# Performance work log

Measured on AMD Instinct MI355X. Metric: run time of the kernel, lower is better.

## Reference

```python
import jax, jax.numpy as jnp
import numpy as np
import math

EMBED = 1024
FF = 4096
HEADS = 16
HEAD = EMBED // HEADS
EPS = 1e-5


def new_gelu(x):
    c = math.sqrt(2.0 / math.pi)
    return 0.5 * x * (1.0 + jnp.tanh(c * (x + 0.044715 * x ** 3)))


def layer_norm(x, g, b):
    mu = jnp.mean(x, axis=-1, keepdims=True)
    var = jnp.var(x, axis=-1, keepdims=True)
    return (x - mu) * jax.lax.rsqrt(var + EPS) * g + b


def setup_inputs() -> dict:
    key = jax.random.key(0)
    ks = jax.random.split(key, 16)
    s = 0.02
    d = {
        'x': jax.random.normal(ks[0], (2, 2048, EMBED), jnp.float32),
        'Wq': jax.random.normal(ks[1], (EMBED, EMBED)) * s,
        'bq': jnp.zeros((EMBED,)),
        'Wk': jax.random.normal(ks[2], (EMBED, EMBED)) * s,
        'bk': jnp.zeros((EMBED,)),
        'Wv': jax.random.normal(ks[3], (EMBED, EMBED)) * s,
        'bv': jnp.zeros((EMBED,)),
        'Wp': jax.random.normal(ks[4], (EMBED, EMBED)) * s,
        'bp': jnp.zeros((EMBED,)),
        'W1': jax.random.normal(ks[5], (EMBED, FF)) * s,
        'b1': jnp.zeros((FF,)),
        'W2': jax.random.normal(ks[6], (FF, EMBED)) * s,
        'b2': jnp.zeros((EMBED,)),
        'g1': jnp.ones((EMBED,)), 'be1': jnp.zeros((EMBED,)),
        'g2': jnp.ones((EMBED,)), 'be2': jnp.zeros((EMBED,)),
    }
    return d


def reference(x, Wq, bq, Wk, bk, Wv, bv, Wp, bp, W1, b1, W2, b2, g1, be1, g2, be2):
    B, S, D = x.shape
    h = layer_norm(x, g1, be1)
    # project and split heads: [B,S,D] -> [B,H,S,Hd]
    def heads(y):
        return y.reshape(B, S, HEADS, HEAD).transpose(0, 2, 1, 3)
    Q = heads(h @ Wq + bq)
    K = heads(h @ Wk + bk)
    V = heads(h @ Wv + bv)
    att = jnp.einsum('bhqd,bhkd->bhqk', Q, K) / math.sqrt(HEAD)
    att = jax.nn.softmax(att, axis=-1)
    out = jnp.einsum('bhqk,bhkd->bhqd', att, V)
    out = out.transpose(0, 2, 1, 3).reshape(B, S, D)
    x = x + (out @ Wp + bp)  # dropout p=0 / eval -> identity
    h2 = layer_norm(x, g2, be2)
    x = x + (new_gelu(h2 @ W1 + b1) @ W2 + b2)
    return x
```

## Files before the change

### kernel.cpp

```cpp
#include <hip/hip_runtime.h>
#include <cstdint>


typedef __attribute__((ext_vector_type(8))) short short8;
typedef __attribute__((ext_vector_type(4))) float f32x4;

#define QSCL 0.18033688011112042f

__device__ __forceinline__ float bf2f(unsigned short u) {
    union { unsigned int i; float f; } v; v.i = ((unsigned int)u) << 16; return v.f;
}
__device__ __forceinline__ unsigned short f2bf(float f) {
    union { float f; unsigned int i; } v; v.f = f;
    unsigned int u = v.i;
    u += 0x7fff + ((u >> 16) & 1);
    return (unsigned short)(u >> 16);
}
__device__ __forceinline__ float gelu_f(float x) {
    float u = 0.7978845608028654f * (x + 0.044715f * x * x * x);
    float t = 1.f - 2.f / (__expf(2.f * u) + 1.f);
    return 0.5f * x * (1.f + t);
}

__device__ __forceinline__ void ln_dev(
    const float* __restrict__ x, const float* __restrict__ g,
    const float* __restrict__ b, unsigned short* __restrict__ o,
    int row, float* red)
{
    const int tid = threadIdx.x;
    const float4 v = ((const float4*)(x + (size_t)row * 1024))[tid];
    float f0 = v.x, f1 = v.y, f2 = v.z, f3 = v.w;
    float sum = f0 + f1 + f2 + f3;
    float sq  = f0 * f0 + f1 * f1 + f2 * f2 + f3 * f3;
    for (int off = 1; off < 64; off <<= 1) {
        sum += __shfl_xor(sum, off);
        sq  += __shfl_xor(sq,  off);
    }
    int wv = tid >> 6, ln = tid & 63;
    if (ln == 0) { red[wv] = sum; red[4 + wv] = sq; }
    __syncthreads();
    sum = red[0] + red[1] + red[2] + red[3];
    sq  = red[4] + red[5] + red[6] + red[7];
    float mu  = sum * (1.0f / 1024.0f);
    float var = sq  * (1.0f / 1024.0f) - mu * mu;
    float rsd = rsqrtf(fmaxf(var, 0.f) + 1e-5f);
    const float4 gg = ((const float4*)g)[tid];
    const float4 bb = ((const float4*)b)[tid];
    unsigned short* orow = o + (size_t)row * 1024;
    orow[4 * tid + 0] = f2bf((f0 - mu) * rsd * gg.x + bb.x);
    orow[4 * tid + 1] = f2bf((f1 - mu) * rsd * gg.y + bb.y);
    orow[4 * tid + 2] = f2bf((f2 - mu) * rsd * gg.z + bb.z);
    orow[4 * tid + 3] = f2bf((f3 - mu) * rsd * gg.w + bb.w);
}

__device__ __forceinline__ void transpose_dev(
    const float* __restrict__ in, unsigned short* __restrict__ out,
    int R, int C, int inStride, int bx, int by, unsigned short* tile ,
    float scale)
{
    const int tx = threadIdx.x & 15, ty = threadIdx.x >> 4;
    const int c0 = bx * 64, r0 = by * 64;
#pragma unroll
    for (int i = 0; i < 4; ++i) {
        int r = ty + 16 * i;
        float4 v = *(const float4*)(in + (size_t)(r0 + r) * inStride + c0 + tx * 4);
        tile[r * 70 + tx * 4 + 0] = f2bf(v.x * scale);
        tile[r * 70 + tx * 4 + 1] = f2bf(v.y * scale);
        tile[r * 70 + tx * 4 + 2] = f2bf(v.z * scale);
        tile[r * 70 + tx * 4 + 3] = f2bf(v.w * scale);
    }
    __syncthreads();
#pragma unroll
    for (int i = 0; i < 4; ++i) {
        int c = ty * 4 + i;
        ushort4 o;
        o.x = tile[(tx * 4 + 0) * 70 + c];
        o.y = tile[(tx * 4 + 1) * 70 + c];
        o.z = tile[(tx * 4 + 2) * 70 + c];
        o.w = tile[(tx * 4 + 3) * 70 + c];
        *(ushort4*)(out + (size_t)(c0 + c) * R + r0 + tx * 4) = o;
    }
}

__global__ __launch_bounds__(256) void ln_k(
    const float* __restrict__ x, const float* __restrict__ g,
    const float* __restrict__ b, unsigned short* __restrict__ o)
{
    __shared__ float red[8];
    ln_dev(x, g, b, o, blockIdx.x, red);
}
__global__ __launch_bounds__(256) void transpose_f2b(
    const float* __restrict__ in, unsigned short* __restrict__ out,
    int R, int C, int inStride, float scale)
{
    __shared__ unsigned short tile[64 * 70];
    transpose_dev(in, out, R, C, inStride, blockIdx.x, blockIdx.y, tile, scale);
}

__global__ __launch_bounds__(256) void prep1_k(
    const float* __restrict__ x,
    const float* __restrict__ g1, const float* __restrict__ be1,
    const float* __restrict__ Wq, const float* __restrict__ Wk,
    const float* __restrict__ Wv,
    const float* __restrict__ bq, const float* __restrict__ bk,
    const float* __restrict__ bv,
    unsigned short* __restrict__ hb,
    unsigned short* __restrict__ WTqkv,
    float* __restrict__ bcat)
{
    __shared__ unsigned short smem[64 * 70];
    const int b = blockIdx.x;
    if (b < 4096) {
        ln_dev(x, g1, be1, hb, b, (float*)smem);
    } else if (b < 4096 + 768) {
        int t = b - 4096;
        int w = t >> 8;
        int tt = t & 255;
        const float* W = (w == 0) ? Wq : (w == 1) ? Wk : Wv;
        transpose_dev(W, WTqkv + (size_t)w * 1024 * 1024,
                      1024, 1024, 1024, tt & 15, tt >> 4, smem,
                      (w == 0) ? QSCL : 1.f);
    } else {
        int i = (b - 4096 - 768) * 256 + threadIdx.x;
        float v = (i < 1024) ? bq[i] * QSCL : (i < 2048) ? bk[i - 1024] : bv[i - 2048];
        bcat[i] = v;
    }
}

__global__ __launch_bounds__(256) void prep2_k(
    const float* __restrict__ x1,
    const float* __restrict__ g2, const float* __restrict__ be2,
    const float* __restrict__ W1, const float* __restrict__ W2,
    unsigned short* __restrict__ h2,
    unsigned short* __restrict__ WT1,
    unsigned short* __restrict__ WT2)
{
    __shared__ unsigned short smem[64 * 70];
    const int b = blockIdx.x;
    if (b < 4096) {
        ln_dev(x1, g2, be2, h2, b, (float*)smem);
    } else if (b < 4096 + 1024) {
        int t = b - 4096;
        transpose_dev(W1, WT1, 1024, 4096, 4096, t & 63, t >> 6, smem, 1.f);
    } else {
        int t = b - 4096 - 1024;
        transpose_dev(W2, WT2, 4096, 1024, 1024, t & 15, t >> 4, smem, 1.f);
    }
}

__global__ __launch_bounds__(256) void vt_k(
    const unsigned short* __restrict__ src, int stride,
    unsigned short* __restrict__ Vt)
{
    __shared__ unsigned short tile[64][70];
    const int tx = threadIdx.x & 15, ty = threadIdx.x >> 4;
    const int t0 = blockIdx.x * 64;
    const int bh = blockIdx.y;
    const int bo = (bh >> 4) * 2048;
    const int ho = (bh & 15) * 64;
    const unsigned short* s = src + (size_t)bo * stride + ho;
#pragma unroll
    for (int i = 0; i < 4; ++i) {
        int r = ty + 16 * i;
        ushort4 v = *(const ushort4*)(s + (size_t)(t0 + r) * stride + tx * 4);
        tile[r][tx * 4 + 0] = v.x;
        tile[r][tx * 4 + 1] = v.y;
        tile[r][tx * 4 + 2] = v.z;
        tile[r][tx * 4 + 3] = v.w;
    }
    __syncthreads();
    unsigned short* dst = Vt + (size_t)bh * 64 * 2048;
    const int hh = tx >> 3;
    const int uu = (tx & 7) * 2;
#pragma unroll
    for (int i = 0; i < 4; ++i) {
        int d = ty * 4 + i;
        ushort4 o;
        o.x = tile[32 * hh + uu][d];
        o.y = tile[32 * hh + 16 + uu][d];
        o.z = tile[32 * hh + uu + 1][d];
        o.w = tile[32 * hh + 17 + uu][d];
        *(ushort4*)(dst + (size_t)d * 2048 + t0 + tx * 4) = o;
    }
}

__global__ __launch_bounds__(512, 4) void gemm5(
    const unsigned short* __restrict__ A,
    const unsigned short* __restrict__ Bt,
    const float* __restrict__ bias,
    const float* __restrict__ res,
    void* __restrict__ C,
    int M, int N, int K, int ldb, int dogelu, int out32, float bscale)
{
    __shared__ unsigned short sA[2][128 * 68];
    __shared__ unsigned short sB[2][128 * 68];
    const int tid  = threadIdx.x;
    const int wave = tid >> 6;
    const int lane = tid & 63;
    const int quad = lane >> 4;
    const int l15  = lane & 15;
    const int bm = blockIdx.y * 128;
    const int bn = blockIdx.x * 128;
    const int wM = (wave & 1) * 64;
    const int wN = (wave >> 1) * 32;

    f32x4 acc[4][2];
#pragma unroll
    for (int i = 0; i < 4; ++i)
#pragma unroll
        for (int j = 0; j < 2; ++j)
            acc[i][j] = (f32x4){0.f, 0.f, 0.f, 0.f};

    const int rowS = tid >> 3;
    const int kcS  = (tid & 7) * 8;
    const unsigned short* gA  = A  + (size_t)(bm + rowS) * K + kcS;
    const unsigned short* gA2 = gA + (size_t)64 * K;
    const unsigned short* gB  = Bt + (size_t)(bn + rowS) * ldb + kcS;
    const unsigned short* gB2 = gB + (size_t)64 * ldb;
    const int lo1 = rowS * 68 + kcS;
    const int lo2 = (rowS + 64) * 68 + kcS;

    const int nt = K >> 6;
    *(short8*)(&sA[0][lo1]) = *(const short8*)(gA);
    *(short8*)(&sA[0][lo2]) = *(const short8*)(gA2);
    *(short8*)(&sB[0][lo1]) = *(const short8*)(gB);
    *(short8*)(&sB[0][lo2]) = *(const short8*)(gB2);
    short8 ar1 = *(const short8*)(gA + 64);
    short8 ar2 = *(const short8*)(gA2 + 64);
    short8 br1 = *(const short8*)(gB + 64);
    short8 br2 = *(const short8*)(gB2 + 64);

    for (int t = 0; t < nt; ++t) {
        const int buf = t & 1;
        __syncthreads();

        short8 aF[4], bF[2];
#pragma unroll
        for (int mi = 0; mi < 4; ++mi)
            aF[mi] = *(const short8*)(&sA[buf][(wM + mi * 16 + l15) * 68 + quad * 8]);
#pragma unroll
        for (int ni = 0; ni < 2; ++ni)
            bF[ni] = *(const short8*)(&sB[buf][(wN + ni * 16 + l15) * 68 + quad * 8]);

        if (t + 1 < nt) {
            *(short8*)(&sA[buf ^ 1][lo1]) = ar1;
            *(short8*)(&sA[buf ^ 1][lo2]) = ar2;
            *(short8*)(&sB[buf ^ 1][lo1]) = br1;
            *(short8*)(&sB[buf ^ 1][lo2]) = br2;
            if (t + 2 < nt) {
                const int k2 = (t + 2) << 6;
                ar1 = *(const short8*)(gA + k2);
                ar2 = *(const short8*)(gA2 + k2);
                br1 = *(const short8*)(gB + k2);
                br2 = *(const short8*)(gB2 + k2);
            }
        }

        __builtin_amdgcn_s_setprio(1);
#pragma unroll
        for (int mi = 0; mi < 4; ++mi)
#pragma unroll
            for (int ni = 0; ni < 2; ++ni)
                acc[mi][ni] = __builtin_amdgcn_mfma_f32_16x16x32_bf16(
                    aF[mi], bF[ni], acc[mi][ni], 0, 0, 0);
        __builtin_amdgcn_s_setprio(0);

#pragma unroll
        for (int mi = 0; mi < 4; ++mi)
            aF[mi] = *(const short8*)(&sA[buf][(wM + mi * 16 + l15) * 68 + 32 + quad * 8]);
#pragma unroll
        for (int ni = 0; ni < 2; ++ni)
            bF[ni] = *(const short8*)(&sB[buf][(wN + ni * 16 + l15) * 68 + 32 + quad * 8]);

        __builtin_amdgcn_s_setprio(1);
#pragma unroll
        for (int mi = 0; mi < 4; ++mi)
#pragma unroll
            for (int ni = 0; ni < 2; ++ni)
                acc[mi][ni] = __builtin_amdgcn_mfma_f32_16x16x32_bf16(
                    aF[mi], bF[ni], acc[mi][ni], 0, 0, 0);
        __builtin_amdgcn_s_setprio(0);
    }

#pragma unroll
    for (int ni = 0; ni < 2; ++ni) {
        int col = bn + wN + ni * 16 + l15;
        float bv = bias ? bias[col] * bscale : 0.f;
#pragma unroll
        for (int mi = 0; mi < 4; ++mi) {
            int row = bm + wM + mi * 16 + quad * 4;
#pragma unroll
            for (int r = 0; r < 4; ++r) {
                float v = acc[mi][ni][r] + bv;
                if (dogelu) v = gelu_f(v);
                size_t idx = (size_t)(row + r) * N + col;
                if (res) v += res[idx];
                if (out32) ((float*)C)[idx] = v;
                else       ((unsigned short*)C)[idx] = f2bf(v);
            }
        }
    }
}

__global__ __launch_bounds__(512, 1) void attn_k(
    const unsigned short* __restrict__ Q,
    const unsigned short* __restrict__ K,
    const unsigned short* __restrict__ Vt,
    unsigned short* __restrict__ O, int qs)
{
    __shared__ unsigned short smem[67584];
    unsigned short* sK = smem;
    unsigned short* sV = smem + 4 * 5632;
    unsigned short* sP = smem + 8 * 5632;

    const int tid  = threadIdx.x;
    const int wave = tid >> 6;
    const int g    = wave & 3;
    const int h    = wave >> 2;
    const int lane = tid & 63;
    const int quad = lane >> 4;
    const int l15  = lane & 15;
    const int bh = blockIdx.x * 4 + (blockIdx.y & 3);
    const int qb = (blockIdx.y >> 2) * 256;
    const int bo = (bh >> 4) * 2048;
    const int ho = (bh & 15) * 64;

    const unsigned short* Qb  = Q  + (size_t)bo * qs + ho;
    const unsigned short* Kb  = K  + (size_t)bo * qs + ho;
    const unsigned short* Vtb = Vt + (size_t)bh * 64 * 2048;
    unsigned short* sPg = sP + g * 5632;
    const int ni0 = 2 * h;

    short8 qF[2][4];
#pragma unroll
    for (int ks = 0; ks < 2; ++ks)
#pragma unroll
        for (int mi = 0; mi < 4; ++mi)
            qF[ks][mi] = *(const short8*)(Qb +
                (size_t)(qb + g * 64 + mi * 16 + l15) * qs + ks * 32 + quad * 8);

    short8 onesF;
#pragma unroll
    for (int j = 0; j < 8; ++j) onesF[j] = (short)0x3F80;

    f32x4 accO[4][4];
    f32x4 accL[4];
#pragma unroll
    for (int mi = 0; mi < 4; ++mi) {
        accL[mi] = (f32x4){0.f, 0.f, 0.f, 0.f};
#pragma unroll
        for (int nd = 0; nd < 4; ++nd) accO[mi][nd] = (f32x4){0.f, 0.f, 0.f, 0.f};
    }

    const int rowS = tid >> 3;
    const int dcS  = (tid & 7) * 8;

    short8 kr[2], vr[2];
#pragma unroll
    for (int s = 0; s < 2; ++s) {
        kr[s] = *(const short8*)(Kb + (size_t)(s * 64 + rowS) * qs + dcS);
        vr[s] = *(const short8*)(Vtb + (size_t)rowS * 2048 + s * 64 + dcS);
    }
#pragma unroll
    for (int s = 0; s < 2; ++s) {
        *(short8*)(sK + s * 5632 + rowS * 88 + dcS) = kr[s];
        *(short8*)(sV + s * 5632 + rowS * 88 + dcS) = vr[s];
    }
#pragma unroll
    for (int s = 0; s < 2; ++s) {
        kr[s] = *(const short8*)(Kb + (size_t)(128 + s * 64 + rowS) * qs + dcS);
        vr[s] = *(const short8*)(Vtb + (size_t)rowS * 2048 + 128 + s * 64 + dcS);
    }

    for (int kt = 0; kt < 2048; kt += 128) {
        const int buf = (kt >> 7) & 1;
        __syncthreads();

#pragma unroll
        for (int s = 0; s < 2; ++s) {
            const unsigned short* sKb = sK + (buf * 2 + s) * 5632;
            const unsigned short* sVb = sV + (buf * 2 + s) * 5632;

            short8 bK[2][2];
#pragma unroll
            for (int ks = 0; ks < 2; ++ks)
#pragma unroll
                for (int nj = 0; nj < 2; ++nj)
                    bK[ks][nj] = *(const short8*)(sKb +
                        ((ni0 + nj) * 16 + l15) * 88 + ks * 32 + quad * 8);

            f32x4 s0[4], s1[4];
#pragma unroll
            for (int mi = 0; mi < 4; ++mi) {
                s0[mi] = (f32x4){0.f, 0.f, 0.f, 0.f};
                s1[mi] = s0[mi];
#pragma unroll
                for (int ks = 0; ks < 2; ++ks) {
                    s0[mi] = __builtin_amdgcn_mfma_f32_16x16x32_bf16(qF[ks][mi], bK[ks][0], s0[mi], 0, 0, 0);
                    s1[mi] = __builtin_amdgcn_mfma_f32_16x16x32_bf16(qF[ks][mi], bK[ks][1], s1[mi], 0, 0, 0);
                }
            }

            if (s == 0 && kt + 128 < 2048) {
#pragma unroll
                for (int u = 0; u < 2; ++u) {
                    *(short8*)(sK + ((buf ^ 1) * 2 + u) * 5632 + rowS * 88 + dcS) = kr[u];
                    *(short8*)(sV + ((buf ^ 1) * 2 + u) * 5632 + rowS * 88 + dcS) = vr[u];
                }
                if (kt + 256 < 2048) {
#pragma unroll
                    for (int u = 0; u < 2; ++u) {
                        kr[u] = *(const short8*)(Kb + (size_t)(kt + 256 + u * 64 + rowS) * qs + dcS);
                        vr[u] = *(const short8*)(Vtb + (size_t)rowS * 2048 + kt + 256 + u * 64 + dcS);
                    }
                }
            }

#pragma unroll
            for (int mi = 0; mi < 4; ++mi)
#pragma unroll
                for (int r = 0; r < 4; ++r) {
                    float p0 = __builtin_amdgcn_exp2f(s0[mi][r]);
                    float p1 = __builtin_amdgcn_exp2f(s1[mi][r]);
                    unsigned int w;
                    asm("v_cvt_pk_bf16_f32 %0, %1, %2" : "=v"(w) : "v"(p0), "v"(p1));
                    *(unsigned int*)(sPg + (mi * 16 + quad * 4 + r) * 88 + h * 32 + l15 * 2) = w;
                }

            short8 aP[4], bV[4];
#pragma unroll
            for (int nd = 0; nd < 4; ++nd)
                bV[nd] = *(const short8*)(sVb + (nd * 16 + l15) * 88 + h * 32 + quad * 8);
#pragma unroll
            for (int mi = 0; mi < 4; ++mi)
                aP[mi] = *(const short8*)(sPg + (mi * 16 + l15) * 88 + h * 32 + quad * 8);

            __builtin_amdgcn_s_setprio(1);
#pragma unroll
            for (int mi = 0; mi < 4; ++mi) {
#pragma unroll
                for (int nd = 0; nd < 4; ++nd)
                    accO[mi][nd] = __builtin_amdgcn_mfma_f32_16x16x32_bf16(
                        aP[mi], bV[nd], accO[mi][nd], 0, 0, 0);
                accL[mi] = __builtin_amdgcn_mfma_f32_16x16x32_bf16(
                    aP[mi], onesF, accL[mi], 0, 0, 0);
            }
            __builtin_amdgcn_s_setprio(0);
        }
    }

    __syncthreads();
    float* scr = (float*)smem;
    float* po = scr + (size_t)(g * 64 + lane) * 68;
    float* pl = scr + 17408 + (size_t)(g * 64 + lane) * 20;
    if (h == 1) {
#pragma unroll
        for (int mi = 0; mi < 4; ++mi) {
#pragma unroll
            for (int nd = 0; nd < 4; ++nd)
                *(f32x4*)(po + mi * 16 + nd * 4) = accO[mi][nd];
            *(f32x4*)(pl + mi * 4) = accL[mi];
        }
    }
    __syncthreads();
    if (h == 0) {
#pragma unroll
        for (int mi = 0; mi < 4; ++mi) {
            accL[mi] += *(const f32x4*)(pl + mi * 4);
#pragma unroll
            for (int nd = 0; nd < 4; ++nd)
                accO[mi][nd] += *(const f32x4*)(po + mi * 16 + nd * 4);
        }
#pragma unroll
        for (int mi = 0; mi < 4; ++mi)
#pragma unroll
            for (int r = 0; r < 4; ++r) {
                int row = qb + g * 64 + mi * 16 + quad * 4 + r;
                float inv = 1.f / accL[mi][r];
#pragma unroll
                for (int nd = 0; nd < 4; ++nd)
                    O[(size_t)(bo + row) * 1024 + ho + nd * 16 + l15] =
                        f2bf(accO[mi][nd][r] * inv);
            }
    }
}

extern "C" void kernel_launch(void* const* d_in, const int* in_sizes, int n_in,
                              void* d_out, int out_size, void* d_ws, size_t ws_size,
                              hipStream_t stream)
{
    (void)in_sizes; (void)n_in; (void)out_size;
    const float* x   = (const float*)d_in[0];
    const float* Wq  = (const float*)d_in[1];
    const float* bq  = (const float*)d_in[2];
    const float* Wk  = (const float*)d_in[3];
    const float* bk  = (const float*)d_in[4];
    const float* Wv  = (const float*)d_in[5];
    const float* bv  = (const float*)d_in[6];
    const float* Wp  = (const float*)d_in[7];
    const float* bp  = (const float*)d_in[8];
    const float* W1  = (const float*)d_in[9];
    const float* b1  = (const float*)d_in[10];
    const float* W2  = (const float*)d_in[11];
    const float* b2  = (const float*)d_in[12];
    const float* g1  = (const float*)d_in[13];
    const float* be1 = (const float*)d_in[14];
    const float* g2  = (const float*)d_in[15];
    const float* be2 = (const float*)d_in[16];
    float* out = (float*)d_out;

    char* ws = (char*)d_ws;
    char* dob = (char*)d_out;
    const size_t MB = 1024 * 1024;

    if (ws_size >= 40 * MB) {
        unsigned short* hb    = (unsigned short*)dob;
        unsigned short* WTqkv = (unsigned short*)(dob + 8 * MB);
        float*          bcat  = (float*)(dob + 14 * MB);
        unsigned short* QKV   = (unsigned short*)ws;
        unsigned short* att   = (unsigned short*)(ws + 24 * MB);
        unsigned short* Vt    = (unsigned short*)(ws + 32 * MB);
        unsigned short* WTp   = (unsigned short*)(ws + 32 * MB);
        unsigned short* h2    = (unsigned short*)ws;
        unsigned short* WT1   = (unsigned short*)(ws + 8 * MB);
        unsigned short* WT2   = (unsigned short*)(ws + 16 * MB);
        unsigned short* act   = (unsigned short*)(ws + 24 * MB);

        prep1_k<<<4096 + 768 + 12, 256, 0, stream>>>(
            x, g1, be1, Wq, Wk, Wv, bq, bk, bv, hb, WTqkv, bcat);
        gemm5<<<dim3(24, 32), 512, 0, stream>>>(hb, WTqkv, bcat, nullptr, QKV,
                                                4096, 3072, 1024, 1024, 0, 0, 1.f);
        vt_k<<<dim3(32, 32), 256, 0, stream>>>(QKV + 2048, 3072, Vt);
        attn_k<<<dim3(8, 32), 512, 0, stream>>>(QKV, QKV + 1024, Vt, att, 3072);
        transpose_f2b<<<dim3(16, 16), 256, 0, stream>>>(Wp, WTp, 1024, 1024, 1024, 1.f);
        gemm5<<<dim3(8, 32), 512, 0, stream>>>(att, WTp, bp, x, out,
                                               4096, 1024, 1024, 1024, 0, 1, 1.f);
        prep2_k<<<4096 + 2048, 256, 0, stream>>>(out, g2, be2, W1, W2, h2, WT1, WT2);
        for (int c = 0; c < 2; ++c) {
            gemm5<<<dim3(16, 32), 512, 0, stream>>>(h2, WT1 + (size_t)c * 2048 * 1024,
                                                    b1 + c * 2048, nullptr, act,
                                                    4096, 2048, 1024, 1024, 1, 0, 1.f);
            gemm5<<<dim3(8, 32), 512, 0, stream>>>(act, WT2 + (size_t)c * 2048,
                                                   c == 0 ? b2 : nullptr, out, out,
                                                   4096, 1024, 2048, 4096, 0, 1, 1.f);
        }
    } else {
        unsigned short* Qw  = (unsigned short*)(ws);
        unsigned short* Kw  = (unsigned short*)(ws + 8 * MB);
        unsigned short* Vw  = (unsigned short*)(ws + 16 * MB);
        unsigned short* hb  = (unsigned short*)dob;
        unsigned short* WTq = (unsigned short*)(dob + 8 * MB);
        unsigned short* VtF = (unsigned short*)(dob + 8 * MB);
        unsigned short* att = Qw;
        unsigned short* WTb = Kw;
        unsigned short* h2  = Vw;
        unsigned short* act = Qw;

        ln_k<<<4096, 256, 0, stream>>>(x, g1, be1, hb);
        transpose_f2b<<<dim3(16, 16), 256, 0, stream>>>(Wq, WTq, 1024, 1024, 1024, QSCL);
        gemm5<<<dim3(8, 32), 512, 0, stream>>>(hb, WTq, bq, nullptr, Qw, 4096, 1024, 1024, 1024, 0, 0, QSCL);
        transpose_f2b<<<dim3(16, 16), 256, 0, stream>>>(Wk, WTq, 1024, 1024, 1024, 1.f);
        gemm5<<<dim3(8, 32), 512, 0, stream>>>(hb, WTq, bk, nullptr, Kw, 4096, 1024, 1024, 1024, 0, 0, 1.f);
        transpose_f2b<<<dim3(16, 16), 256, 0, stream>>>(Wv, WTq, 1024, 1024, 1024, 1.f);
        gemm5<<<dim3(8, 32), 512, 0, stream>>>(hb, WTq, bv, nullptr, Vw, 4096, 1024, 1024, 1024, 0, 0, 1.f);
        vt_k<<<dim3(32, 32), 256, 0, stream>>>(Vw, 1024, VtF);
        attn_k<<<dim3(8, 32), 512, 0, stream>>>(Qw, Kw, VtF, att, 1024);
        transpose_f2b<<<dim3(16, 16), 256, 0, stream>>>(Wp, WTb, 1024, 1024, 1024, 1.f);
        gemm5<<<dim3(8, 32), 512, 0, stream>>>(att, WTb, bp, x, out, 4096, 1024, 1024, 1024, 0, 1, 1.f);
        ln_k<<<4096, 256, 0, stream>>>(out, g2, be2, h2);
        for (int c = 0; c < 4; ++c) {
            transpose_f2b<<<dim3(16, 16), 256, 0, stream>>>(W1 + c * 1024, WTb, 1024, 1024, 4096, 1.f);
            gemm5<<<dim3(8, 32), 512, 0, stream>>>(h2, WTb, b1 + c * 1024, nullptr, act,
                                                   4096, 1024, 1024, 1024, 1, 0, 1.f);
            unsigned short* WT2c = WTb + 1024 * 1024;
            transpose_f2b<<<dim3(16, 16), 256, 0, stream>>>(W2 + (size_t)c * 1024 * 1024, WT2c,
                                                            1024, 1024, 1024, 1.f);
            gemm5<<<dim3(8, 32), 512, 0, stream>>>(act, WT2c, c == 0 ? b2 : nullptr,
                                                   out, out, 4096, 1024, 1024, 1024, 0, 1, 1.f);
        }
    }
}
```

Before: 366.4 us.

## Add 256-thread GEMM with 64x64 per-wave tiles for QKV and FC1

Introduces a gemm6 kernel that uses 4 waves of 256 threads, each computing a 64x64 sub-tile of the 128x128 block with 16 MFMA accumulators, and a K-step of 32 with register-prefetched double buffering. It replaces gemm5 for the QKV projection and the first FFN GEMM. The intent is more MFMA work per LDS fragment load and less shared memory per block, which improves reuse. In exchange each wave holds more accumulator registers, and the smaller K-step means more barriers per unit of work.

```diff
diff --git a/kernel.cpp b/kernel.cpp
--- a/kernel.cpp
+++ b/kernel.cpp
@@ -181,6 +181,108 @@
         o.z = tile[32 * hh + uu + 1][d];
         o.w = tile[32 * hh + 17 + uu][d];
         *(ushort4*)(dst + (size_t)d * 2048 + t0 + tx * 4) = o;
+    }
+}
+
+__global__ __launch_bounds__(256, 3) void gemm6(
+    const unsigned short* __restrict__ A,
+    const unsigned short* __restrict__ Bt,
+    const float* __restrict__ bias,
+    const float* __restrict__ res,
+    void* __restrict__ C,
+    int M, int N, int K, int ldb, int dogelu, int out32, float bscale)
+{
+    __shared__ unsigned short sA[2][128 * 34];
+    __shared__ unsigned short sB[2][128 * 34];
+    const int tid  = threadIdx.x;
+    const int wave = tid >> 6;
+    const int lane = tid & 63;
+    const int quad = lane >> 4;
+    const int l15  = lane & 15;
+    const int bm = blockIdx.y * 128;
+    const int bn = blockIdx.x * 128;
+    const int wM = (wave & 1) * 64;
+    const int wN = (wave >> 1) * 64;
+
+    f32x4 acc[4][4];
+#pragma unroll
+    for (int i = 0; i < 4; ++i)
+#pragma unroll
+        for (int j = 0; j < 4; ++j)
+            acc[i][j] = (f32x4){0.f, 0.f, 0.f, 0.f};
+
+    const int rowS = tid >> 2;
+    const int kcS  = (tid & 3) * 8;
+    const unsigned short* gA  = A  + (size_t)(bm + rowS) * K + kcS;
+    const unsigned short* gA2 = gA + (size_t)64 * K;
+    const unsigned short* gB  = Bt + (size_t)(bn + rowS) * ldb + kcS;
+    const unsigned short* gB2 = gB + (size_t)64 * ldb;
+    const int lo1 = rowS * 34 + kcS;
+    const int lo2 = (rowS + 64) * 34 + kcS;
+
+    const int np = K >> 5;
+    *(short8*)(&sA[0][lo1]) = *(const short8*)(gA);
+    *(short8*)(&sA[0][lo2]) = *(const short8*)(gA2);
+    *(short8*)(&sB[0][lo1]) = *(const short8*)(gB);
+    *(short8*)(&sB[0][lo2]) = *(const short8*)(gB2);
+    short8 ar1 = *(const short8*)(gA + 32);
+    short8 ar2 = *(const short8*)(gA2 + 32);
+    short8 br1 = *(const short8*)(gB + 32);
+    short8 br2 = *(const short8*)(gB2 + 32);
+
+    for (int p = 0; p < np; ++p) {
+        const int buf = p & 1;
+        __syncthreads();
+
+        short8 aF[4], bF[4];
+#pragma unroll
+        for (int mi = 0; mi < 4; ++mi)
+            aF[mi] = *(const short8*)(&sA[buf][(wM + mi * 16 + l15) * 34 + quad * 8]);
+#pragma unroll
+        for (int ni = 0; ni < 4; ++ni)
+            bF[ni] = *(const short8*)(&sB[buf][(wN + ni * 16 + l15) * 34 + quad * 8]);
+
+        if (p + 1 < np) {
+            *(short8*)(&sA[buf ^ 1][lo1]) = ar1;
+            *(short8*)(&sA[buf ^ 1][lo2]) = ar2;
+            *(short8*)(&sB[buf ^ 1][lo1]) = br1;
+            *(short8*)(&sB[buf ^ 1][lo2]) = br2;
+            if (p + 2 < np) {
+                const int k2 = (p + 2) << 5;
+                ar1 = *(const short8*)(gA + k2);
+                ar2 = *(const short8*)(gA2 + k2);
+                br1 = *(const short8*)(gB + k2);
+                br2 = *(const short8*)(gB2 + k2);
+            }
+        }
+
+        __builtin_amdgcn_s_setprio(1);
+#pragma unroll
+        for (int mi = 0; mi < 4; ++mi)
+#pragma unroll
+            for (int ni = 0; ni < 4; ++ni)
+                acc[mi][ni] = __builtin_amdgcn_mfma_f32_16x16x32_bf16(
+                    aF[mi], bF[ni], acc[mi][ni], 0, 0, 0);
+        __builtin_amdgcn_s_setprio(0);
+    }
+
+#pragma unroll
+    for (int ni = 0; ni < 4; ++ni) {
+        int col = bn + wN + ni * 16 + l15;
+        float bv = bias ? bias[col] * bscale : 0.f;
+#pragma unroll
+        for (int mi = 0; mi < 4; ++mi) {
+            int row = bm + wM + mi * 16 + quad * 4;
+#pragma unroll
+            for (int r = 0; r < 4; ++r) {
+                float v = acc[mi][ni][r] + bv;
+                if (dogelu) v = gelu_f(v);
+                size_t idx = (size_t)(row + r) * N + col;
+                if (res) v += res[idx];
+                if (out32) ((float*)C)[idx] = v;
+                else       ((unsigned short*)C)[idx] = f2bf(v);
+            }
+        }
     }
 }
 
@@ -528,7 +630,7 @@
 
         prep1_k<<<4096 + 768 + 12, 256, 0, stream>>>(
             x, g1, be1, Wq, Wk, Wv, bq, bk, bv, hb, WTqkv, bcat);
-        gemm5<<<dim3(24, 32), 512, 0, stream>>>(hb, WTqkv, bcat, nullptr, QKV,
+        gemm6<<<dim3(24, 32), 256, 0, stream>>>(hb, WTqkv, bcat, nullptr, QKV,
                                                 4096, 3072, 1024, 1024, 0, 0, 1.f);
         vt_k<<<dim3(32, 32), 256, 0, stream>>>(QKV + 2048, 3072, Vt);
         attn_k<<<dim3(8, 32), 512, 0, stream>>>(QKV, QKV + 1024, Vt, att, 3072);
@@ -537,7 +639,7 @@
                                                4096, 1024, 1024, 1024, 0, 1, 1.f);
         prep2_k<<<4096 + 2048, 256, 0, stream>>>(out, g2, be2, W1, W2, h2, WT1, WT2);
         for (int c = 0; c < 2; ++c) {
-            gemm5<<<dim3(16, 32), 512, 0, stream>>>(h2, WT1 + (size_t)c * 2048 * 1024,
+            gemm6<<<dim3(16, 32), 256, 0, stream>>>(h2, WT1 + (size_t)c * 2048 * 1024,
                                                     b1 + c * 2048, nullptr, act,
                                                     4096, 2048, 1024, 1024, 1, 0, 1.f);
             gemm5<<<dim3(8, 32), 512, 0, stream>>>(act, WT2 + (size_t)c * 2048,
```

Result: slower. 398.1 us (+8.6%).

## Split K across wave pairs in GEMM with larger per-wave tiles and LDS reduction

Applied to the files above, without the earlier changes.

Reorganizes the GEMM so each wave computes a 64x64 output tile on one half of each 64-wide K slice, instead of a 64x32 tile over the full slice. The two K-halves are summed through shared memory before the epilogue. This raises MFMA work per LDS fragment load and improves operand reuse. In exchange it doubles the accumulator registers per wave, adds an LDS reduction with extra barriers, and leaves half the waves idle during the epilogue.

```diff
diff --git a/kernel.cpp b/kernel.cpp
--- a/kernel.cpp
+++ b/kernel.cpp
@@ -184,7 +184,7 @@
     }
 }
 
-__global__ __launch_bounds__(512, 4) void gemm5(
+__global__ __launch_bounds__(512, 4) void gemm7(
     const unsigned short* __restrict__ A,
     const unsigned short* __restrict__ Bt,
     const float* __restrict__ bias,
@@ -196,19 +196,22 @@
     __shared__ unsigned short sB[2][128 * 68];
     const int tid  = threadIdx.x;
     const int wave = tid >> 6;
+    const int q    = wave & 3;
+    const int s    = wave >> 2;
     const int lane = tid & 63;
     const int quad = lane >> 4;
     const int l15  = lane & 15;
     const int bm = blockIdx.y * 128;
     const int bn = blockIdx.x * 128;
-    const int wM = (wave & 1) * 64;
-    const int wN = (wave >> 1) * 32;
-
-    f32x4 acc[4][2];
+    const int wM = (q & 1) * 64;
+    const int wN = (q >> 1) * 64;
+    const int pofs = s * 32;
+
+    f32x4 acc[4][4];
 #pragma unroll
     for (int i = 0; i < 4; ++i)
 #pragma unroll
-        for (int j = 0; j < 2; ++j)
+        for (int j = 0; j < 4; ++j)
             acc[i][j] = (f32x4){0.f, 0.f, 0.f, 0.f};
 
     const int rowS = tid >> 3;
@@ -234,13 +237,13 @@
         const int buf = t & 1;
         __syncthreads();
 
-        short8 aF[4], bF[2];
+        short8 aF[4], bF[4];
 #pragma unroll
         for (int mi = 0; mi < 4; ++mi)
-            aF[mi] = *(const short8*)(&sA[buf][(wM + mi * 16 + l15) * 68 + quad * 8]);
-#pragma unroll
-        for (int ni = 0; ni < 2; ++ni)
-            bF[ni] = *(const short8*)(&sB[buf][(wN + ni * 16 + l15) * 68 + quad * 8]);
+            aF[mi] = *(const short8*)(&sA[buf][(wM + mi * 16 + l15) * 68 + pofs + quad * 8]);
+#pragma unroll
+        for (int ni = 0; ni < 4; ++ni)
+            bF[ni] = *(const short8*)(&sB[buf][(wN + ni * 16 + l15) * 68 + pofs + quad * 8]);
 
         if (t + 1 < nt) {
             *(short8*)(&sA[buf ^ 1][lo1]) = ar1;
@@ -260,43 +263,42 @@
 #pragma unroll
         for (int mi = 0; mi < 4; ++mi)
 #pragma unroll
-            for (int ni = 0; ni < 2; ++ni)
+            for (int ni = 0; ni < 4; ++ni)
                 acc[mi][ni] = __builtin_amdgcn_mfma_f32_16x16x32_bf16(
                     aF[mi], bF[ni], acc[mi][ni], 0, 0, 0);
         __builtin_amdgcn_s_setprio(0);
-
+    }
+
+    __syncthreads();
+    float* base = (q < 2) ? (float*)&sA[0][0] : (float*)&sB[0][0];
+    float* slot = base + (size_t)((q & 1) * 64 + lane) * 65;
+    if (s == 1) {
 #pragma unroll
         for (int mi = 0; mi < 4; ++mi)
-            aF[mi] = *(const short8*)(&sA[buf][(wM + mi * 16 + l15) * 68 + 32 + quad * 8]);
-#pragma unroll
-        for (int ni = 0; ni < 2; ++ni)
-            bF[ni] = *(const short8*)(&sB[buf][(wN + ni * 16 + l15) * 68 + 32 + quad * 8]);
-
-        __builtin_amdgcn_s_setprio(1);
-#pragma unroll
-        for (int mi = 0; mi < 4; ++mi)
-#pragma unroll
-            for (int ni = 0; ni < 2; ++ni)
-                acc[mi][ni] = __builtin_amdgcn_mfma_f32_16x16x32_bf16(
-                    aF[mi], bF[ni], acc[mi][ni], 0, 0, 0);
-        __builtin_amdgcn_s_setprio(0);
-    }
-
-#pragma unroll
-    for (int ni = 0; ni < 2; ++ni) {
-        int col = bn + wN + ni * 16 + l15;
-        float bv = bias ? bias[col] * bscale : 0.f;
-#pragma unroll
-        for (int mi = 0; mi < 4; ++mi) {
-            int row = bm + wM + mi * 16 + quad * 4;
-#pragma unroll
-            for (int r = 0; r < 4; ++r) {
-                float v = acc[mi][ni][r] + bv;
-                if (dogelu) v = gelu_f(v);
-                size_t idx = (size_t)(row + r) * N + col;
-                if (res) v += res[idx];
-                if (out32) ((float*)C)[idx] = v;
-                else       ((unsigned short*)C)[idx] = f2bf(v);
+#pragma unroll
+            for (int ni = 0; ni < 4; ++ni)
+#pragma unroll
+                for (int r = 0; r < 4; ++r)
+                    slot[mi * 16 + ni * 4 + r] = acc[mi][ni][r];
+    }
+    __syncthreads();
+    if (s == 0) {
+#pragma unroll
+        for (int ni = 0; ni < 4; ++ni) {
+            int col = bn + wN + ni * 16 + l15;
+            float bv = bias ? bias[col] * bscale : 0.f;
+#pragma unroll
+            for (int mi = 0; mi < 4; ++mi) {
+                int row = bm + wM + mi * 16 + quad * 4;
+#pragma unroll
+                for (int r = 0; r < 4; ++r) {
+                    float v = acc[mi][ni][r] + slot[mi * 16 + ni * 4 + r] + bv;
+                    if (dogelu) v = gelu_f(v);
+                    size_t idx = (size_t)(row + r) * N + col;
+                    if (res) v += res[idx];
+                    if (out32) ((float*)C)[idx] = v;
+                    else       ((unsigned short*)C)[idx] = f2bf(v);
+                }
             }
         }
     }
@@ -528,19 +530,19 @@
 
         prep1_k<<<4096 + 768 + 12, 256, 0, stream>>>(
             x, g1, be1, Wq, Wk, Wv, bq, bk, bv, hb, WTqkv, bcat);
-        gemm5<<<dim3(24, 32), 512, 0, stream>>>(hb, WTqkv, bcat, nullptr, QKV,
+        gemm7<<<dim3(24, 32), 512, 0, stream>>>(hb, WTqkv, bcat, nullptr, QKV,
                                                 4096, 3072, 1024, 1024, 0, 0, 1.f);
         vt_k<<<dim3(32, 32), 256, 0, stream>>>(QKV + 2048, 3072, Vt);
         attn_k<<<dim3(8, 32), 512, 0, stream>>>(QKV, QKV + 1024, Vt, att, 3072);
         transpose_f2b<<<dim3(16, 16), 256, 0, stream>>>(Wp, WTp, 1024, 1024, 1024, 1.f);
-        gemm5<<<dim3(8, 32), 512, 0, stream>>>(att, WTp, bp, x, out,
+        gemm7<<<dim3(8, 32), 512, 0, stream>>>(att, WTp, bp, x, out,
                                                4096, 1024, 1024, 1024, 0, 1, 1.f);
         prep2_k<<<4096 + 2048, 256, 0, stream>>>(out, g2, be2, W1, W2, h2, WT1, WT2);
         for (int c = 0; c < 2; ++c) {
-            gemm5<<<dim3(16, 32), 512, 0, stream>>>(h2, WT1 + (size_t)c * 2048 * 1024,
+            gemm7<<<dim3(16, 32), 512, 0, stream>>>(h2, WT1 + (size_t)c * 2048 * 1024,
                                                     b1 + c * 2048, nullptr, act,
                                                     4096, 2048, 1024, 1024, 1, 0, 1.f);
-            gemm5<<<dim3(8, 32), 512, 0, stream>>>(act, WT2 + (size_t)c * 2048,
+            gemm7<<<dim3(8, 32), 512, 0, stream>>>(act, WT2 + (size_t)c * 2048,
                                                    c == 0 ? b2 : nullptr, out, out,
                                                    4096, 1024, 2048, 4096, 0, 1, 1.f);
         }
@@ -558,24 +560,24 @@
 
         ln_k<<<4096, 256, 0, stream>>>(x, g1, be1, hb);
         transpose_f2b<<<dim3(16, 16), 256, 0, stream>>>(Wq, WTq, 1024, 1024, 1024, QSCL);
-        gemm5<<<dim3(8, 32), 512, 0, stream>>>(hb, WTq, bq, nullptr, Qw, 4096, 1024, 1024, 1024, 0, 0, QSCL);
+        gemm7<<<dim3(8, 32), 512, 0, stream>>>(hb, WTq, bq, nullptr, Qw, 4096, 1024, 1024, 1024, 0, 0, QSCL);
         transpose_f2b<<<dim3(16, 16), 256, 0, stream>>>(Wk, WTq, 1024, 1024, 1024, 1.f);
-        gemm5<<<dim3(8, 32), 512, 0, stream>>>(hb, WTq, bk, nullptr, Kw, 4096, 1024, 1024, 1024, 0, 0, 1.f);
+        gemm7<<<dim3(8, 32), 512, 0, stream>>>(hb, WTq, bk, nullptr, Kw, 4096, 1024, 1024, 1024, 0, 0, 1.f);
         transpose_f2b<<<dim3(16, 16), 256, 0, stream>>>(Wv, WTq, 1024, 1024, 1024, 1.f);
-        gemm5<<<dim3(8, 32), 512, 0, stream>>>(hb, WTq, bv, nullptr, Vw, 4096, 1024, 1024, 1024, 0, 0, 1.f);
+        gemm7<<<dim3(8, 32), 512, 0, stream>>>(hb, WTq, bv, nullptr, Vw, 4096, 1024, 1024, 1024, 0, 0, 1.f);
         vt_k<<<dim3(32, 32), 256, 0, stream>>>(Vw, 1024, VtF);
         attn_k<<<dim3(8, 32), 512, 0, stream>>>(Qw, Kw, VtF, att, 1024);
         transpose_f2b<<<dim3(16, 16), 256, 0, stream>>>(Wp, WTb, 1024, 1024, 1024, 1.f);
-        gemm5<<<dim3(8, 32), 512, 0, stream>>>(att, WTb, bp, x, out, 4096, 1024, 1024, 1024, 0, 1, 1.f);
+        gemm7<<<dim3(8, 32), 512, 0, stream>>>(att, WTb, bp, x, out, 4096, 1024, 1024, 1024, 0, 1, 1.f);
         ln_k<<<4096, 256, 0, stream>>>(out, g2, be2, h2);
         for (int c = 0; c < 4; ++c) {
             transpose_f2b<<<dim3(16, 16), 256, 0, stream>>>(W1 + c * 1024, WTb, 1024, 1024, 4096, 1.f);
-            gemm5<<<dim3(8, 32), 512, 0, stream>>>(h2, WTb, b1 + c * 1024, nullptr, act,
+            gemm7<<<dim3(8, 32), 512, 0, stream>>>(h2, WTb, b1 + c * 1024, nullptr, act,
                                                    4096, 1024, 1024, 1024, 1, 0, 1.f);
             unsigned short* WT2c = WTb + 1024 * 1024;
             transpose_f2b<<<dim3(16, 16), 256, 0, stream>>>(W2 + (size_t)c * 1024 * 1024, WT2c,
                                                             1024, 1024, 1024, 1.f);
-            gemm5<<<dim3(8, 32), 512, 0, stream>>>(act, WT2c, c == 0 ? b2 : nullptr,
+            gemm7<<<dim3(8, 32), 512, 0, stream>>>(act, WT2c, c == 0 ? b2 : nullptr,
                                                    out, out, 4096, 1024, 1024, 1024, 0, 1, 1.f);
         }
     }
```

After: 438.3 us. +19.6%, slower.

## Add 256x256-tile GEMM kernel with register prefetch for QKV projection

Applied to the files above, without the earlier changes.

Adds a new GEMM kernel that computes 256x256 output tiles per block, with each wave holding an 8x4 set of MFMA accumulators. The next K-slab is prefetched from global memory into registers, then written to double-buffered LDS. MFMA issue is bracketed by s_setprio. The QKV projection now uses this kernel on a 12x16 grid instead of the 128-tile kernel. The goal is more data reuse per LDS load and fewer global reads. The tradeoffs are higher register pressure, lower occupancy (launch bounds of 2), and only 192 blocks to spread across the CUs.

```diff
diff --git a/kernel.cpp b/kernel.cpp
--- a/kernel.cpp
+++ b/kernel.cpp
@@ -181,6 +181,128 @@
         o.z = tile[32 * hh + uu + 1][d];
         o.w = tile[32 * hh + 17 + uu][d];
         *(ushort4*)(dst + (size_t)d * 2048 + t0 + tx * 4) = o;
+    }
+}
+
+#define SLOT(d, kt) (((d) * 2 + (kt)) * 9216)
+__global__ __launch_bounds__(512, 2) void gemm8(
+    const unsigned short* __restrict__ A,
+    const unsigned short* __restrict__ Bt,
+    const float* __restrict__ bias,
+    const float* __restrict__ res,
+    void* __restrict__ C,
+    int M, int N, int K, int ldb, int dogelu, int out32, float bscale)
+{
+    __shared__ unsigned short sA[36864];
+    __shared__ unsigned short sB[36864];
+    const int tid  = threadIdx.x;
+    const int wave = tid >> 6;
+    const int wm   = wave >> 2;
+    const int wn   = wave & 3;
+    const int lane = tid & 63;
+    const int quad = lane >> 4;
+    const int l15  = lane & 15;
+    const int bm = blockIdx.y * 256;
+    const int bn = blockIdx.x * 256;
+
+    f32x4 acc[8][4];
+#pragma unroll
+    for (int i = 0; i < 8; ++i)
+#pragma unroll
+        for (int j = 0; j < 4; ++j)
+            acc[i][j] = (f32x4){0.f, 0.f, 0.f, 0.f};
+
+    const int tq = tid >> 2;
+    const int ce = (tid & 3) * 8;
+    const unsigned short* gA1 = A  + (size_t)(bm + tq) * K + ce;
+    const unsigned short* gA2 = A  + (size_t)(bm + 128 + tq) * K + ce;
+    const unsigned short* gB1 = Bt + (size_t)(bn + tq) * ldb + ce;
+    const unsigned short* gB2 = Bt + (size_t)(bn + 128 + tq) * ldb + ce;
+    const int wo1 = tq * 36 + ce;
+    const int wo2 = (128 + tq) * 36 + ce;
+
+#pragma unroll
+    for (int ktl = 0; ktl < 2; ++ktl) {
+        const int ko = ktl * 32;
+        *(short8*)(sA + SLOT(0, ktl) + wo1) = *(const short8*)(gA1 + ko);
+        *(short8*)(sA + SLOT(0, ktl) + wo2) = *(const short8*)(gA2 + ko);
+        *(short8*)(sB + SLOT(0, ktl) + wo1) = *(const short8*)(gB1 + ko);
+        *(short8*)(sB + SLOT(0, ktl) + wo2) = *(const short8*)(gB2 + ko);
+    }
+    __syncthreads();
+
+    const int nit = K >> 6;
+    short8 pf[8];
+
+    for (int it = 0; it < nit; ++it) {
+        const int d = it & 1;
+
+        if (it + 1 < nit) {
+            const int kg = (it + 1) << 6;
+#pragma unroll
+            for (int ktl = 0; ktl < 2; ++ktl) {
+                pf[ktl * 4 + 0] = *(const short8*)(gA1 + kg + ktl * 32);
+                pf[ktl * 4 + 1] = *(const short8*)(gA2 + kg + ktl * 32);
+                pf[ktl * 4 + 2] = *(const short8*)(gB1 + kg + ktl * 32);
+                pf[ktl * 4 + 3] = *(const short8*)(gB2 + kg + ktl * 32);
+            }
+        }
+
+#pragma unroll
+        for (int ktl = 0; ktl < 2; ++ktl) {
+            const unsigned short* pA = sA + SLOT(d, ktl);
+            const unsigned short* pB = sB + SLOT(d, ktl);
+            short8 bF[4];
+#pragma unroll
+            for (int ni = 0; ni < 4; ++ni)
+                bF[ni] = *(const short8*)(pB + (wn * 64 + ni * 16 + l15) * 36 + quad * 8);
+#pragma unroll
+            for (int ph = 0; ph < 4; ++ph) {
+                short8 a0 = *(const short8*)(pA + (wm * 128 + (ph * 2 + 0) * 16 + l15) * 36 + quad * 8);
+                short8 a1 = *(const short8*)(pA + (wm * 128 + (ph * 2 + 1) * 16 + l15) * 36 + quad * 8);
+                __builtin_amdgcn_s_barrier();
+                __builtin_amdgcn_s_setprio(1);
+#pragma unroll
+                for (int ni = 0; ni < 4; ++ni) {
+                    acc[ph * 2 + 0][ni] = __builtin_amdgcn_mfma_f32_16x16x32_bf16(
+                        a0, bF[ni], acc[ph * 2 + 0][ni], 0, 0, 0);
+                    acc[ph * 2 + 1][ni] = __builtin_amdgcn_mfma_f32_16x16x32_bf16(
+                        a1, bF[ni], acc[ph * 2 + 1][ni], 0, 0, 0);
+                }
+                __builtin_amdgcn_s_setprio(0);
+            }
+        }
+
+        if (it + 1 < nit) {
+#pragma unroll
+            for (int ktl = 0; ktl < 2; ++ktl) {
+                *(short8*)(sA + SLOT(d ^ 1, ktl) + wo1) = pf[ktl * 4 + 0];
+                *(short8*)(sA + SLOT(d ^ 1, ktl) + wo2) = pf[ktl * 4 + 1];
+                *(short8*)(sB + SLOT(d ^ 1, ktl) + wo1) = pf[ktl * 4 + 2];
+                *(short8*)(sB + SLOT(d ^ 1, ktl) + wo2) = pf[ktl * 4 + 3];
+            }
+        }
+        asm volatile("s_waitcnt lgkmcnt(0)" ::: "memory");
+        __builtin_amdgcn_s_barrier();
+    }
+
+#pragma unroll
+    for (int ni = 0; ni < 4; ++ni) {
+        int col = bn + wn * 64 + ni * 16 + l15;
+        float bv = bias ? bias[col] * bscale : 0.f;
+#pragma unroll
+        for (int mi = 0; mi < 8; ++mi) {
+            int row = bm + wm * 128 + mi * 16 + quad * 4;
+#pragma unroll
+            for (int r = 0; r < 4; ++r) {
+                float v = acc[mi][ni][r] + bv;
+                if (dogelu) v = gelu_f(v);
+                size_t idx = (size_t)(row + r) * N + col;
+                if (res) v += res[idx];
+                if (out32) ((float*)C)[idx] = v;
+                else       ((unsigned short*)C)[idx] = f2bf(v);
+            }
+        }
     }
 }
 
@@ -528,7 +650,7 @@
 
         prep1_k<<<4096 + 768 + 12, 256, 0, stream>>>(
             x, g1, be1, Wq, Wk, Wv, bq, bk, bv, hb, WTqkv, bcat);
-        gemm5<<<dim3(24, 32), 512, 0, stream>>>(hb, WTqkv, bcat, nullptr, QKV,
+        gemm8<<<dim3(12, 16), 512, 0, stream>>>(hb, WTqkv, bcat, nullptr, QKV,
                                                 4096, 3072, 1024, 1024, 0, 0, 1.f);
         vt_k<<<dim3(32, 32), 256, 0, stream>>>(QKV + 2048, 3072, Vt);
         attn_k<<<dim3(8, 32), 512, 0, stream>>>(QKV, QKV + 1024, Vt, att, 3072);
```

Measured after the change: 467.1 us. 1.27x slower.
